# Kernel optimization log

Measured on AMD Instinct MI355X. Metric: run time of the kernel, lower is better.

## Reference

```python
import jax, jax.numpy as jnp
import numpy as np

HID = 256
DT = 0.05
B = 131072


def setup_inputs() -> dict:
    key = jax.random.key(0)
    ks = jax.random.split(key, 20)
    n = jax.random.normal
    inp = {
        "q": n(ks[0], (B, 1), jnp.float32),
        "p": n(ks[1], (B, 1), jnp.float32),
        "u": n(ks[2], (B, 1), jnp.float32),
        # kinetic MLP T(q_enc, p): in dim 3
        "kW1": n(ks[3], (HID, 3), jnp.float32) / np.sqrt(3.0),
        "kb1": n(ks[4], (HID,), jnp.float32) * 0.01,
        "kW2": n(ks[5], (HID, HID), jnp.float32) / np.sqrt(HID),
        "kb2": n(ks[6], (HID,), jnp.float32) * 0.01,
        "kW3": n(ks[7], (1, HID), jnp.float32) / np.sqrt(HID),
        "kb3": n(ks[8], (1,), jnp.float32) * 0.01,
        # potential MLP V(q_enc): in dim 2
        "pW1": n(ks[9], (HID, 2), jnp.float32) / np.sqrt(2.0),
        "pb1": n(ks[10], (HID,), jnp.float32) * 0.01,
        "pW2": n(ks[11], (HID, HID), jnp.float32) / np.sqrt(HID),
        "pb2": n(ks[12], (HID,), jnp.float32) * 0.01,
        "pW3": n(ks[13], (1, HID), jnp.float32) / np.sqrt(HID),
        "pb3": n(ks[14], (1,), jnp.float32) * 0.01,
        # learned structure matrices (std=0.01 as in nn.init.normal_)
        "A": n(ks[15], (2, 2), jnp.float32) * 0.01,
        "L_param": n(ks[16], (2, 2), jnp.float32) * 0.01,
        "b_ctrl": n(ks[17], (1, 1), jnp.float32) * 0.01,
    }
    return inp


def reference(q, p, u, kW1, kb1, kW2, kb2, kW3, kb3,
              pW1, pb1, pW2, pb2, pW3, pb3, A, L_param, b_ctrl):
    sp = jax.nn.softplus

    def H_sum(z):  # z: [B,2] -> scalar sum of H over batch
        q_, p_ = z[:, :1], z[:, 1:]
        enc = jnp.concatenate([jnp.sin(q_), jnp.cos(q_)], axis=-1)  # [B,2]
        x = jnp.concatenate([enc, p_], axis=-1)                      # [B,3]
        h = sp(x @ kW1.T + kb1)
        h = sp(h @ kW2.T + kb2)
        T = (h @ kW3.T + kb3)[:, 0]
        g = sp(enc @ pW1.T + pb1)
        g = sp(g @ pW2.T + pb2)
        V = (g @ pW3.T + pb3)[:, 0]
        return jnp.sum(T + V)

    # M = J - R with J = A - A^T, R = L L^T, L = strict-lower + softplus(diag)
    J = A - A.T
    L = jnp.tril(L_param, -1) + jnp.diag(sp(jnp.diagonal(L_param)))
    M = J - L @ L.T                          # [2,2]
    Bu = u @ b_ctrl.T                        # [B,1]
    zeros_q = jnp.zeros_like(q)

    def dyn(q_, p_):
        # torch detaches z before autograd.grad -> stop_gradient here
        z = jax.lax.stop_gradient(jnp.concatenate([q_, p_], axis=-1))
        gH = jax.grad(H_sum)(z)              # [B,2] = dH/dz per sample
        dz = gH @ M.T + jnp.concatenate([zeros_q, Bu], axis=-1)
        return dz[:, :1], dz[:, 1:]

    dt = DT
    dq1, dp1 = dyn(q, p)
    dq2, dp2 = dyn(q + 0.5 * dt * dq1, p + 0.5 * dt * dp1)
    dq3, dp3 = dyn(q + 0.5 * dt * dq2, p + 0.5 * dt * dp2)
    dq4, dp4 = dyn(q + dt * dq3, p + dt * dp3)
    q_next = q + dt / 6.0 * (dq1 + 2 * dq2 + 2 * dq3 + dq4)
    p_next = p + dt / 6.0 * (dp1 + 2 * dp2 + 2 * dp3 + dp4)
    return jnp.concatenate([q_next, p_next], axis=-1)  # [B,2]
```

## Files before the change

### kernel.cpp

```cpp
#include <hip/hip_runtime.h>

#define HID 256
#define BT 64
#define DTC 0.05f

typedef __attribute__((ext_vector_type(4))) float f32x4;
typedef __attribute__((ext_vector_type(8))) __bf16 bf16x8;

__device__ __forceinline__ unsigned cvt_pk_bf16(float lo, float hi) {
    unsigned r;
    asm("v_cvt_pk_bf16_f32 %0, %1, %2" : "=v"(r) : "v"(lo), "v"(hi));
    return r;
}

__device__ __forceinline__ unsigned short f2bf(float f) {
    unsigned int x = __float_as_uint(f);
    x += 0x7fffu + ((x >> 16) & 1u);
    return (unsigned short)(x >> 16);
}

__device__ __forceinline__ float sgpr_f(float v) {
    return __uint_as_float(__builtin_amdgcn_readfirstlane(__float_as_uint(v)));
}

#define OFF_FWDT 0
#define OFF_BWDT 65536
#define OFF_FWDV 131072
#define OFF_BWDV 196608
#define OFF_PROJT 262144
#define OFF_PROJV 266240
#define TOTAL_PRE 270336

__global__ void prepack_kernel(const float* __restrict__ kW1, const float* __restrict__ kW2,
                               const float* __restrict__ pW1, const float* __restrict__ pW2,
                               unsigned short* __restrict__ ws) {
    int t = blockIdx.x * 256 + threadIdx.x;
    if (t >= TOTAL_PRE) return;
    float v;
    if (t < OFF_FWDV) {
        int tt = t & 65535;
        bool bwd = t >= OFF_BWDT;
        int j = tt & 7, lane = (tt >> 3) & 63, kk = (tt >> 9) & 7, nt = tt >> 12;
        int n = nt * 16 + (lane & 15);
        int k = kk * 32 + (lane >> 4) * 8 + j;
        v = bwd ? kW2[k * HID + n] : kW2[n * HID + k];
    } else if (t < OFF_PROJT) {
        int tt = (t - OFF_FWDV) & 65535;
        bool bwd = t >= OFF_BWDV;
        int j = tt & 7, lane = (tt >> 3) & 63, kk = (tt >> 9) & 7, nt = tt >> 12;
        int n = nt * 16 + (lane & 15);
        int k = kk * 32 + (lane >> 4) * 8 + j;
        v = bwd ? pW2[k * HID + n] : pW2[n * HID + k];
    } else if (t < OFF_PROJV) {
        int tt = t - OFF_PROJT;
        int j = tt & 7, lane = (tt >> 3) & 63, kk = tt >> 9;
        int c = lane & 15;
        int k = kk * 32 + (lane >> 4) * 8 + j;
        v = (c < 3) ? kW1[k * 3 + c] : 0.f;
    } else {
        int tt = t - OFF_PROJV;
        int j = tt & 7, lane = (tt >> 3) & 63, kk = tt >> 9;
        int c = lane & 15;
        int k = kk * 32 + (lane >> 4) * 8 + j;
        v = (c < 2) ? pW1[k * 2 + c] : 0.f;
    }
    ws[t] = f2bf(v);
}


#define MFMA __builtin_amdgcn_mfma_f32_16x16x32_bf16

struct NetRegs { float w0[2], w1[2], w2[2], b1[2], b2[2], w3[2]; };

template <int IND, int NOUT>
__device__ __forceinline__ void run_net(
    char* bufAc, char* bufBc,
    const float* sh_sin, const float* sh_cos, const float* sh_pv,
    const NetRegs& R,
    const unsigned short* __restrict__ fwdB, const unsigned short* __restrict__ bwdB,
    const unsigned short* __restrict__ projB,
    float* g0, float* g1, float* g2,
    int w, int lane)
{
    const int lr = lane & 15;
    const int lg = lane >> 4;
    const unsigned int arx = (unsigned)(lr & 7) << 4;
    const unsigned int cbase = ((unsigned)lg << 4) ^ arx;

    unsigned s1p[16];

#pragma unroll
    for (int mt = 0; mt < 4; ++mt) {
#pragma unroll
        for (int r = 0; r < 4; ++r) {
            int row = mt * 16 + lg * 4 + r;
            float sv = sh_sin[row], cv = sh_cos[row];
            float pv = (IND == 3) ? sh_pv[row] : 0.f;
            unsigned int rowx = (unsigned)(row & 7) << 4;
            char* rowp = bufAc + row * 512;
            float sp[2], sg[2];
#pragma unroll
            for (int nt = 0; nt < 2; ++nt) {
                float x = fmaf(R.w0[nt], sv, R.b1[nt]);
                x = fmaf(R.w1[nt], cv, x);
                if (IND == 3) x = fmaf(R.w2[nt], pv, x);
                float e = __expf(-fabsf(x));
                sp[nt] = fmaxf(x, 0.f) + __logf(1.f + e);
                float t = __builtin_amdgcn_rcpf(1.f + e);
                sg[nt] = (x < 0.f) ? e * t : t;
            }
            unsigned d01 = cvt_pk_bf16(sp[0], sp[1]);
            int j0 = w * 32 + lr;
            *(unsigned short*)(rowp + (((j0 +  0) * 2) ^ rowx)) = (unsigned short)d01;
            *(unsigned short*)(rowp + (((j0 + 16) * 2) ^ rowx)) = (unsigned short)(d01 >> 16);
            s1p[mt * 4 + r] = cvt_pk_bf16(sg[0], sg[1]);
        }
    }

    const unsigned short* fb = fwdB + (w * 2) * 8 * 512 + lane * 8;
    bf16x8 c0 = *(const bf16x8*)(fb + 0 * 512);
    bf16x8 c1 = *(const bf16x8*)(fb + 8 * 512);
    __syncthreads();

    f32x4 acc[4][2];
#pragma unroll
    for (int mt = 0; mt < 4; ++mt)
#pragma unroll
        for (int nt = 0; nt < 2; ++nt)
            acc[mt][nt] = (f32x4){0.f, 0.f, 0.f, 0.f};
    {
#pragma unroll 1
        for (int kk = 0; kk < 8; ++kk) {
            unsigned int off = cbase ^ (unsigned)(kk << 6);
            bf16x8 af0 = *(const bf16x8*)(bufAc + (0 * 16 + lr) * 512 + off);
            bf16x8 af1 = *(const bf16x8*)(bufAc + (1 * 16 + lr) * 512 + off);
            bf16x8 af2 = *(const bf16x8*)(bufAc + (2 * 16 + lr) * 512 + off);
            bf16x8 af3 = *(const bf16x8*)(bufAc + (3 * 16 + lr) * 512 + off);
            acc[0][0] = MFMA(af0, c0, acc[0][0], 0, 0, 0);
            acc[0][1] = MFMA(af0, c1, acc[0][1], 0, 0, 0);
            acc[1][0] = MFMA(af1, c0, acc[1][0], 0, 0, 0);
            acc[1][1] = MFMA(af1, c1, acc[1][1], 0, 0, 0);
            acc[2][0] = MFMA(af2, c0, acc[2][0], 0, 0, 0);
            acc[2][1] = MFMA(af2, c1, acc[2][1], 0, 0, 0);
            acc[3][0] = MFMA(af3, c0, acc[3][0], 0, 0, 0);
            acc[3][1] = MFMA(af3, c1, acc[3][1], 0, 0, 0);
            if (kk < 7) {
                c0 = *(const bf16x8*)(fb + (0 * 8 + kk + 1) * 512);
                c1 = *(const bf16x8*)(fb + (1 * 8 + kk + 1) * 512);
            }
        }
    }

#pragma unroll
    for (int nt = 0; nt < 2; ++nt) {
        int i = w * 32 + nt * 16 + lr;
#pragma unroll
        for (int mt = 0; mt < 4; ++mt) {
            float val[4];
#pragma unroll
            for (int r = 0; r < 4; ++r) {
                float x = acc[mt][nt][r] + R.b2[nt];
                float e = __expf(-fabsf(x));
                float t = __builtin_amdgcn_rcpf(1.f + e);
                float sg = (x < 0.f) ? e * t : t;
                val[r] = R.w3[nt] * sg;
            }
            unsigned d01 = cvt_pk_bf16(val[0], val[1]);
            unsigned d23 = cvt_pk_bf16(val[2], val[3]);
#pragma unroll
            for (int r = 0; r < 4; ++r) {
                int row = mt * 16 + lg * 4 + r;
                unsigned short hv = (r == 0) ? (unsigned short)d01
                                  : (r == 1) ? (unsigned short)(d01 >> 16)
                                  : (r == 2) ? (unsigned short)d23
                                             : (unsigned short)(d23 >> 16);
                *(unsigned short*)(bufBc + row * 512 + ((i * 2) ^ ((unsigned)(row & 7) << 4))) = hv;
            }
        }
    }

    const unsigned short* bb = bwdB + (w * 2) * 8 * 512 + lane * 8;
    c0 = *(const bf16x8*)(bb + 0 * 512);
    c1 = *(const bf16x8*)(bb + 8 * 512);
    __syncthreads();

#pragma unroll
    for (int mt = 0; mt < 4; ++mt)
#pragma unroll
        for (int nt = 0; nt < 2; ++nt)
            acc[mt][nt] = (f32x4){0.f, 0.f, 0.f, 0.f};
    {
#pragma unroll 1
        for (int kk = 0; kk < 8; ++kk) {
            unsigned int off = cbase ^ (unsigned)(kk << 6);
            bf16x8 af0 = *(const bf16x8*)(bufBc + (0 * 16 + lr) * 512 + off);
            bf16x8 af1 = *(const bf16x8*)(bufBc + (1 * 16 + lr) * 512 + off);
            bf16x8 af2 = *(const bf16x8*)(bufBc + (2 * 16 + lr) * 512 + off);
            bf16x8 af3 = *(const bf16x8*)(bufBc + (3 * 16 + lr) * 512 + off);
            acc[0][0] = MFMA(af0, c0, acc[0][0], 0, 0, 0);
            acc[0][1] = MFMA(af0, c1, acc[0][1], 0, 0, 0);
            acc[1][0] = MFMA(af1, c0, acc[1][0], 0, 0, 0);
            acc[1][1] = MFMA(af1, c1, acc[1][1], 0, 0, 0);
            acc[2][0] = MFMA(af2, c0, acc[2][0], 0, 0, 0);
            acc[2][1] = MFMA(af2, c1, acc[2][1], 0, 0, 0);
            acc[3][0] = MFMA(af3, c0, acc[3][0], 0, 0, 0);
            acc[3][1] = MFMA(af3, c1, acc[3][1], 0, 0, 0);
            if (kk < 7) {
                c0 = *(const bf16x8*)(bb + (0 * 8 + kk + 1) * 512);
                c1 = *(const bf16x8*)(bb + (1 * 8 + kk + 1) * 512);
            }
        }
    }

#pragma unroll
    for (int mt = 0; mt < 4; ++mt) {
#pragma unroll
        for (int r = 0; r < 4; ++r) {
            int row = mt * 16 + lg * 4 + r;
            unsigned int rowx = (unsigned)(row & 7) << 4;
            char* rowp = bufAc + row * 512;
            unsigned pa = s1p[mt * 4 + r];
            float sg0 = __uint_as_float(pa << 16);
            float sg1 = __uint_as_float(pa & 0xffff0000u);
            unsigned d01 = cvt_pk_bf16(acc[mt][0][r] * sg0, acc[mt][1][r] * sg1);
            int j0 = w * 32 + lr;
            *(unsigned short*)(rowp + (((j0 +  0) * 2) ^ rowx)) = (unsigned short)d01;
            *(unsigned short*)(rowp + (((j0 + 16) * 2) ^ rowx)) = (unsigned short)(d01 >> 16);
        }
    }
    __syncthreads();

    if (w < 4) {
        const unsigned short* pb = projB + lane * 8;
        f32x4 pacc = (f32x4){0.f, 0.f, 0.f, 0.f};
        char* arow = bufAc + (w * 16 + lr) * 512;
#pragma unroll 1
        for (int kk = 0; kk < 8; ++kk) {
            bf16x8 bv = *(const bf16x8*)(pb + kk * 512);
            bf16x8 af = *(const bf16x8*)(arow + (cbase ^ (unsigned)(kk << 6)));
            pacc = MFMA(af, bv, pacc, 0, 0, 0);
        }
        if (lr < NOUT) {
            float* dst = (lr == 0) ? g0 : ((lr == 1) ? g1 : g2);
#pragma unroll
            for (int r = 0; r < 4; ++r) dst[w * 16 + lg * 4 + r] = pacc[r];
        }
    }
    __syncthreads();
}

__global__ __launch_bounds__(512, 2) void phgn_kernel(
    const float* __restrict__ q, const float* __restrict__ p, const float* __restrict__ u,
    const float* __restrict__ kW1, const float* __restrict__ kb1,
    const float* __restrict__ kb2, const float* __restrict__ kW3,
    const float* __restrict__ pW1, const float* __restrict__ pb1,
    const float* __restrict__ pb2, const float* __restrict__ pW3,
    const float* __restrict__ A, const float* __restrict__ Lp, const float* __restrict__ bctrl,
    const unsigned short* __restrict__ ws, float* __restrict__ out)
{
    __shared__ __attribute__((aligned(16))) unsigned short bufA[BT * HID];
    __shared__ __attribute__((aligned(16))) unsigned short bufB[BT * HID];
    __shared__ float sh_sin[BT], sh_cos[BT], sh_pv[BT];
    __shared__ float gx0[BT], gx1[BT], gx2[BT], ge0[BT], ge1[BT];

    const int tid = threadIdx.x;
    const int w = tid >> 6, lane = tid & 63;
    const int lr = lane & 15;
    const int base = blockIdx.x * BT;

    NetRegs RT, RV;
#pragma unroll
    for (int nt = 0; nt < 2; ++nt) {
        int j = w * 32 + nt * 16 + lr;
        RT.w0[nt] = kW1[j * 3 + 0];
        RT.w1[nt] = kW1[j * 3 + 1];
        RT.w2[nt] = kW1[j * 3 + 2];
        RT.b1[nt] = kb1[j];
        RT.b2[nt] = kb2[j];
        RT.w3[nt] = kW3[j];
        RV.w0[nt] = pW1[j * 2 + 0];
        RV.w1[nt] = pW1[j * 2 + 1];
        RV.w2[nt] = 0.f;
        RV.b1[nt] = pb1[j];
        RV.b2[nt] = pb2[j];
        RV.w3[nt] = pW3[j];
    }

    float l00 = __logf(1.f + __expf(Lp[0]));
    float l11 = __logf(1.f + __expf(Lp[3]));
    float l10 = Lp[2];
    float J01 = A[1] - A[2];
    float M00 = sgpr_f(-(l00 * l00));
    float M01 = sgpr_f(J01 - l00 * l10);
    float M10 = sgpr_f(-J01 - l10 * l00);
    float M11 = sgpr_f(-(l10 * l10 + l11 * l11));

    float q0 = 0.f, p0 = 0.f, buv = 0.f, aq = 0.f, ap = 0.f;
    if (tid < BT) {
        q0 = q[base + tid]; p0 = p[base + tid]; buv = u[base + tid] * bctrl[0];
        float s, c; __sincosf(q0, &s, &c);
        sh_sin[tid] = s; sh_cos[tid] = c; sh_pv[tid] = p0;
    }
    __syncthreads();

    char* bufAc = (char*)bufA;
    char* bufBc = (char*)bufB;
#pragma unroll 1
    for (int s = 0; s < 4; ++s) {
        run_net<3, 3>(bufAc, bufBc, sh_sin, sh_cos, sh_pv, RT,
                      ws + OFF_FWDT, ws + OFF_BWDT, ws + OFF_PROJT, gx0, gx1, gx2, w, lane);
        run_net<2, 2>(bufAc, bufBc, sh_sin, sh_cos, sh_pv, RV,
                      ws + OFF_FWDV, ws + OFF_BWDV, ws + OFF_PROJV, ge0, ge1, ge1, w, lane);
        if (tid < BT) {
            float gq = (gx0[tid] + ge0[tid]) * sh_cos[tid] - (gx1[tid] + ge1[tid]) * sh_sin[tid];
            float gp = gx2[tid];
            float dq = M00 * gq + M01 * gp;
            float dp = M10 * gq + M11 * gp + buv;
            float wgt = (s == 0 || s == 3) ? 1.f : 2.f;
            aq += wgt * dq; ap += wgt * dp;
            if (s < 3) {
                float cs = (s == 2) ? 1.f : 0.5f;
                float qs = fmaf(cs * DTC, dq, q0);
                float ps = fmaf(cs * DTC, dp, p0);
                float sn, cn; __sincosf(qs, &sn, &cn);
                sh_sin[tid] = sn; sh_cos[tid] = cn; sh_pv[tid] = ps;
            } else {
                float qn = fmaf(DTC / 6.f, aq, q0);
                float pn = fmaf(DTC / 6.f, ap, p0);
                ((float2*)out)[base + tid] = make_float2(qn, pn);
            }
        }
        __syncthreads();
    }
}

extern "C" void kernel_launch(void* const* d_in, const int* in_sizes, int n_in,
                              void* d_out, int out_size, void* d_ws, size_t ws_size,
                              hipStream_t stream) {
    const float* q    = (const float*)d_in[0];
    const float* p    = (const float*)d_in[1];
    const float* u    = (const float*)d_in[2];
    const float* kW1  = (const float*)d_in[3];
    const float* kb1  = (const float*)d_in[4];
    const float* kW2  = (const float*)d_in[5];
    const float* kb2  = (const float*)d_in[6];
    const float* kW3  = (const float*)d_in[7];
    const float* pW1  = (const float*)d_in[9];
    const float* pb1  = (const float*)d_in[10];
    const float* pW2  = (const float*)d_in[11];
    const float* pb2  = (const float*)d_in[12];
    const float* pW3  = (const float*)d_in[13];
    const float* A    = (const float*)d_in[15];
    const float* Lp   = (const float*)d_in[16];
    const float* bctl = (const float*)d_in[17];
    unsigned short* ws = (unsigned short*)d_ws;
    float* out = (float*)d_out;
    int B = in_sizes[0];

    prepack_kernel<<<(TOTAL_PRE + 255) / 256, 256, 0, stream>>>(kW1, kW2, pW1, pW2, ws);
    phgn_kernel<<<B / BT, 512, 0, stream>>>(q, p, u, kW1, kb1, kb2, kW3,
                                            pW1, pb1, pb2, pW3, A, Lp, bctl, ws, out);
}
```

Baseline: 715.2 us.

## Split batch rows across two wave groups with 1024-thread blocks

Doubles the block from 8 to 16 waves. Each wave now owns a 32-row by 32-column tile instead of 64 rows by 32 columns, with `wm` selecting the row half and `wn` the column slice. This halves per-wave accumulators and MFMA work and raises the resident wave count, to hide LDS and exp latency. In exchange, more waves contend at each `__syncthreads`, and the B fragments are loaded redundantly by both row groups. The tighter launch bounds may also force register spills or limit occupancy through the 64 KB of LDS per block.

```diff
diff --git a/kernel.cpp b/kernel.cpp
--- a/kernel.cpp
+++ b/kernel.cpp
@@ -80,20 +80,20 @@
     const unsigned short* __restrict__ fwdB, const unsigned short* __restrict__ bwdB,
     const unsigned short* __restrict__ projB,
     float* g0, float* g1, float* g2,
-    int w, int lane)
+    int wm, int wn, int w, int lane)
 {
     const int lr = lane & 15;
     const int lg = lane >> 4;
     const unsigned int arx = (unsigned)(lr & 7) << 4;
     const unsigned int cbase = ((unsigned)lg << 4) ^ arx;
 
-    unsigned s1p[16];
-
-#pragma unroll
-    for (int mt = 0; mt < 4; ++mt) {
+    unsigned s1p[8];
+
+#pragma unroll
+    for (int mt = 0; mt < 2; ++mt) {
 #pragma unroll
         for (int r = 0; r < 4; ++r) {
-            int row = mt * 16 + lg * 4 + r;
+            int row = wm * 32 + mt * 16 + lg * 4 + r;
             float sv = sh_sin[row], cv = sh_cos[row];
             float pv = (IND == 3) ? sh_pv[row] : 0.f;
             unsigned int rowx = (unsigned)(row & 7) << 4;
@@ -110,21 +110,21 @@
                 sg[nt] = (x < 0.f) ? e * t : t;
             }
             unsigned d01 = cvt_pk_bf16(sp[0], sp[1]);
-            int j0 = w * 32 + lr;
+            int j0 = wn * 32 + lr;
             *(unsigned short*)(rowp + (((j0 +  0) * 2) ^ rowx)) = (unsigned short)d01;
             *(unsigned short*)(rowp + (((j0 + 16) * 2) ^ rowx)) = (unsigned short)(d01 >> 16);
             s1p[mt * 4 + r] = cvt_pk_bf16(sg[0], sg[1]);
         }
     }
 
-    const unsigned short* fb = fwdB + (w * 2) * 8 * 512 + lane * 8;
+    const unsigned short* fb = fwdB + (wn * 2) * 8 * 512 + lane * 8;
     bf16x8 c0 = *(const bf16x8*)(fb + 0 * 512);
     bf16x8 c1 = *(const bf16x8*)(fb + 8 * 512);
     __syncthreads();
 
-    f32x4 acc[4][2];
-#pragma unroll
-    for (int mt = 0; mt < 4; ++mt)
+    f32x4 acc[2][2];
+#pragma unroll
+    for (int mt = 0; mt < 2; ++mt)
 #pragma unroll
         for (int nt = 0; nt < 2; ++nt)
             acc[mt][nt] = (f32x4){0.f, 0.f, 0.f, 0.f};
@@ -132,18 +132,12 @@
 #pragma unroll 1
         for (int kk = 0; kk < 8; ++kk) {
             unsigned int off = cbase ^ (unsigned)(kk << 6);
-            bf16x8 af0 = *(const bf16x8*)(bufAc + (0 * 16 + lr) * 512 + off);
-            bf16x8 af1 = *(const bf16x8*)(bufAc + (1 * 16 + lr) * 512 + off);
-            bf16x8 af2 = *(const bf16x8*)(bufAc + (2 * 16 + lr) * 512 + off);
-            bf16x8 af3 = *(const bf16x8*)(bufAc + (3 * 16 + lr) * 512 + off);
+            bf16x8 af0 = *(const bf16x8*)(bufAc + (wm * 32 +  0 + lr) * 512 + off);
+            bf16x8 af1 = *(const bf16x8*)(bufAc + (wm * 32 + 16 + lr) * 512 + off);
             acc[0][0] = MFMA(af0, c0, acc[0][0], 0, 0, 0);
             acc[0][1] = MFMA(af0, c1, acc[0][1], 0, 0, 0);
             acc[1][0] = MFMA(af1, c0, acc[1][0], 0, 0, 0);
             acc[1][1] = MFMA(af1, c1, acc[1][1], 0, 0, 0);
-            acc[2][0] = MFMA(af2, c0, acc[2][0], 0, 0, 0);
-            acc[2][1] = MFMA(af2, c1, acc[2][1], 0, 0, 0);
-            acc[3][0] = MFMA(af3, c0, acc[3][0], 0, 0, 0);
-            acc[3][1] = MFMA(af3, c1, acc[3][1], 0, 0, 0);
             if (kk < 7) {
                 c0 = *(const bf16x8*)(fb + (0 * 8 + kk + 1) * 512);
                 c1 = *(const bf16x8*)(fb + (1 * 8 + kk + 1) * 512);
@@ -153,9 +147,9 @@
 
 #pragma unroll
     for (int nt = 0; nt < 2; ++nt) {
-        int i = w * 32 + nt * 16 + lr;
-#pragma unroll
-        for (int mt = 0; mt < 4; ++mt) {
+        int i = wn * 32 + nt * 16 + lr;
+#pragma unroll
+        for (int mt = 0; mt < 2; ++mt) {
             float val[4];
 #pragma unroll
             for (int r = 0; r < 4; ++r) {
@@ -169,7 +163,7 @@
             unsigned d23 = cvt_pk_bf16(val[2], val[3]);
 #pragma unroll
             for (int r = 0; r < 4; ++r) {
-                int row = mt * 16 + lg * 4 + r;
+                int row = wm * 32 + mt * 16 + lg * 4 + r;
                 unsigned short hv = (r == 0) ? (unsigned short)d01
                                   : (r == 1) ? (unsigned short)(d01 >> 16)
                                   : (r == 2) ? (unsigned short)d23
@@ -179,13 +173,13 @@
         }
     }
 
-    const unsigned short* bb = bwdB + (w * 2) * 8 * 512 + lane * 8;
+    const unsigned short* bb = bwdB + (wn * 2) * 8 * 512 + lane * 8;
     c0 = *(const bf16x8*)(bb + 0 * 512);
     c1 = *(const bf16x8*)(bb + 8 * 512);
     __syncthreads();
 
 #pragma unroll
-    for (int mt = 0; mt < 4; ++mt)
+    for (int mt = 0; mt < 2; ++mt)
 #pragma unroll
         for (int nt = 0; nt < 2; ++nt)
             acc[mt][nt] = (f32x4){0.f, 0.f, 0.f, 0.f};
@@ -193,18 +187,12 @@
 #pragma unroll 1
         for (int kk = 0; kk < 8; ++kk) {
             unsigned int off = cbase ^ (unsigned)(kk << 6);
-            bf16x8 af0 = *(const bf16x8*)(bufBc + (0 * 16 + lr) * 512 + off);
-            bf16x8 af1 = *(const bf16x8*)(bufBc + (1 * 16 + lr) * 512 + off);
-            bf16x8 af2 = *(const bf16x8*)(bufBc + (2 * 16 + lr) * 512 + off);
-            bf16x8 af3 = *(const bf16x8*)(bufBc + (3 * 16 + lr) * 512 + off);
+            bf16x8 af0 = *(const bf16x8*)(bufBc + (wm * 32 +  0 + lr) * 512 + off);
+            bf16x8 af1 = *(const bf16x8*)(bufBc + (wm * 32 + 16 + lr) * 512 + off);
             acc[0][0] = MFMA(af0, c0, acc[0][0], 0, 0, 0);
             acc[0][1] = MFMA(af0, c1, acc[0][1], 0, 0, 0);
             acc[1][0] = MFMA(af1, c0, acc[1][0], 0, 0, 0);
             acc[1][1] = MFMA(af1, c1, acc[1][1], 0, 0, 0);
-            acc[2][0] = MFMA(af2, c0, acc[2][0], 0, 0, 0);
-            acc[2][1] = MFMA(af2, c1, acc[2][1], 0, 0, 0);
-            acc[3][0] = MFMA(af3, c0, acc[3][0], 0, 0, 0);
-            acc[3][1] = MFMA(af3, c1, acc[3][1], 0, 0, 0);
             if (kk < 7) {
                 c0 = *(const bf16x8*)(bb + (0 * 8 + kk + 1) * 512);
                 c1 = *(const bf16x8*)(bb + (1 * 8 + kk + 1) * 512);
@@ -213,17 +201,17 @@
     }
 
 #pragma unroll
-    for (int mt = 0; mt < 4; ++mt) {
+    for (int mt = 0; mt < 2; ++mt) {
 #pragma unroll
         for (int r = 0; r < 4; ++r) {
-            int row = mt * 16 + lg * 4 + r;
+            int row = wm * 32 + mt * 16 + lg * 4 + r;
             unsigned int rowx = (unsigned)(row & 7) << 4;
             char* rowp = bufAc + row * 512;
             unsigned pa = s1p[mt * 4 + r];
             float sg0 = __uint_as_float(pa << 16);
             float sg1 = __uint_as_float(pa & 0xffff0000u);
             unsigned d01 = cvt_pk_bf16(acc[mt][0][r] * sg0, acc[mt][1][r] * sg1);
-            int j0 = w * 32 + lr;
+            int j0 = wn * 32 + lr;
             *(unsigned short*)(rowp + (((j0 +  0) * 2) ^ rowx)) = (unsigned short)d01;
             *(unsigned short*)(rowp + (((j0 + 16) * 2) ^ rowx)) = (unsigned short)(d01 >> 16);
         }
@@ -249,7 +237,7 @@
     __syncthreads();
 }
 
-__global__ __launch_bounds__(512, 2) void phgn_kernel(
+__global__ __launch_bounds__(1024, 4) void phgn_kernel(
     const float* __restrict__ q, const float* __restrict__ p, const float* __restrict__ u,
     const float* __restrict__ kW1, const float* __restrict__ kb1,
     const float* __restrict__ kb2, const float* __restrict__ kW3,
@@ -265,13 +253,14 @@
 
     const int tid = threadIdx.x;
     const int w = tid >> 6, lane = tid & 63;
+    const int wm = w >> 3, wn = w & 7;
     const int lr = lane & 15;
     const int base = blockIdx.x * BT;
 
     NetRegs RT, RV;
 #pragma unroll
     for (int nt = 0; nt < 2; ++nt) {
-        int j = w * 32 + nt * 16 + lr;
+        int j = wn * 32 + nt * 16 + lr;
         RT.w0[nt] = kW1[j * 3 + 0];
         RT.w1[nt] = kW1[j * 3 + 1];
         RT.w2[nt] = kW1[j * 3 + 2];
@@ -308,9 +297,9 @@
 #pragma unroll 1
     for (int s = 0; s < 4; ++s) {
         run_net<3, 3>(bufAc, bufBc, sh_sin, sh_cos, sh_pv, RT,
-                      ws + OFF_FWDT, ws + OFF_BWDT, ws + OFF_PROJT, gx0, gx1, gx2, w, lane);
+                      ws + OFF_FWDT, ws + OFF_BWDT, ws + OFF_PROJT, gx0, gx1, gx2, wm, wn, w, lane);
         run_net<2, 2>(bufAc, bufBc, sh_sin, sh_cos, sh_pv, RV,
-                      ws + OFF_FWDV, ws + OFF_BWDV, ws + OFF_PROJV, ge0, ge1, ge1, w, lane);
+                      ws + OFF_FWDV, ws + OFF_BWDV, ws + OFF_PROJV, ge0, ge1, ge1, wm, wn, w, lane);
         if (tid < BT) {
             float gq = (gx0[tid] + ge0[tid]) * sh_cos[tid] - (gx1[tid] + ge1[tid]) * sh_sin[tid];
             float gp = gx2[tid];
@@ -358,6 +347,6 @@
     int B = in_sizes[0];
 
     prepack_kernel<<<(TOTAL_PRE + 255) / 256, 256, 0, stream>>>(kW1, kW2, pW1, pW2, ws);
-    phgn_kernel<<<B / BT, 512, 0, stream>>>(q, p, u, kW1, kb1, kb2, kW3,
-                                            pW1, pb1, pb2, pW3, A, Lp, bctl, ws, out);
-}
+    phgn_kernel<<<B / BT, 1024, 0, stream>>>(q, p, u, kW1, kb1, kb2, kW3,
+                                             pW1, pb1, pb2, pW3, A, Lp, bctl, ws, out);
+}
```

Result: slower. 807.2 us (+12.9%).

## Permute K dimension in prepacked weights to enable packed 32-bit LDS stores

Applied to the files above, without the earlier changes.

Reorders the K index in the prepacked weight layouts so that each lane's two hidden columns (j and j+16) sit adjacent in the activation rows. The three LDS writes of activations can then store one 32-bit packed bf16 pair instead of two 16-bit halves, halving LDS store instructions. The per-row sin/cos/p loads also become 16-byte vector reads from aligned shared arrays. The permutation must stay consistent across all MFMA operand layouts, which adds correctness risk.

```diff
diff --git a/kernel.cpp b/kernel.cpp
--- a/kernel.cpp
+++ b/kernel.cpp
@@ -42,26 +42,30 @@
         bool bwd = t >= OFF_BWDT;
         int j = tt & 7, lane = (tt >> 3) & 63, kk = (tt >> 9) & 7, nt = tt >> 12;
         int n = nt * 16 + (lane & 15);
-        int k = kk * 32 + (lane >> 4) * 8 + j;
+        int p = (lane >> 4) * 8 + j;
+        int k = kk * 32 + ((p & 1) << 4) + (p >> 1);
         v = bwd ? kW2[k * HID + n] : kW2[n * HID + k];
     } else if (t < OFF_PROJT) {
         int tt = (t - OFF_FWDV) & 65535;
         bool bwd = t >= OFF_BWDV;
         int j = tt & 7, lane = (tt >> 3) & 63, kk = (tt >> 9) & 7, nt = tt >> 12;
         int n = nt * 16 + (lane & 15);
-        int k = kk * 32 + (lane >> 4) * 8 + j;
+        int p = (lane >> 4) * 8 + j;
+        int k = kk * 32 + ((p & 1) << 4) + (p >> 1);
         v = bwd ? pW2[k * HID + n] : pW2[n * HID + k];
     } else if (t < OFF_PROJV) {
         int tt = t - OFF_PROJT;
         int j = tt & 7, lane = (tt >> 3) & 63, kk = tt >> 9;
         int c = lane & 15;
-        int k = kk * 32 + (lane >> 4) * 8 + j;
+        int p = (lane >> 4) * 8 + j;
+        int k = kk * 32 + ((p & 1) << 4) + (p >> 1);
         v = (c < 3) ? kW1[k * 3 + c] : 0.f;
     } else {
         int tt = t - OFF_PROJV;
         int j = tt & 7, lane = (tt >> 3) & 63, kk = tt >> 9;
         int c = lane & 15;
-        int k = kk * 32 + (lane >> 4) * 8 + j;
+        int p = (lane >> 4) * 8 + j;
+        int k = kk * 32 + ((p & 1) << 4) + (p >> 1);
         v = (c < 2) ? pW1[k * 2 + c] : 0.f;
     }
     ws[t] = f2bf(v);
@@ -86,18 +90,21 @@
     const int lg = lane >> 4;
     const unsigned int arx = (unsigned)(lr & 7) << 4;
     const unsigned int cbase = ((unsigned)lg << 4) ^ arx;
+    const unsigned int colb = (unsigned)(w * 64 + lr * 4);
 
     unsigned s1p[16];
 
 #pragma unroll
     for (int mt = 0; mt < 4; ++mt) {
+        int r0 = mt * 16 + lg * 4;
+        f32x4 sv4 = *(const f32x4*)&sh_sin[r0];
+        f32x4 cv4 = *(const f32x4*)&sh_cos[r0];
+        f32x4 pv4 = *(const f32x4*)&sh_pv[r0];
 #pragma unroll
         for (int r = 0; r < 4; ++r) {
-            int row = mt * 16 + lg * 4 + r;
-            float sv = sh_sin[row], cv = sh_cos[row];
-            float pv = (IND == 3) ? sh_pv[row] : 0.f;
-            unsigned int rowx = (unsigned)(row & 7) << 4;
-            char* rowp = bufAc + row * 512;
+            int row = r0 + r;
+            float sv = sv4[r], cv = cv4[r];
+            float pv = (IND == 3) ? pv4[r] : 0.f;
             float sp[2], sg[2];
 #pragma unroll
             for (int nt = 0; nt < 2; ++nt) {
@@ -109,11 +116,9 @@
                 float t = __builtin_amdgcn_rcpf(1.f + e);
                 sg[nt] = (x < 0.f) ? e * t : t;
             }
-            unsigned d01 = cvt_pk_bf16(sp[0], sp[1]);
-            int j0 = w * 32 + lr;
-            *(unsigned short*)(rowp + (((j0 +  0) * 2) ^ rowx)) = (unsigned short)d01;
-            *(unsigned short*)(rowp + (((j0 + 16) * 2) ^ rowx)) = (unsigned short)(d01 >> 16);
+            unsigned dsp = cvt_pk_bf16(sp[0], sp[1]);
             s1p[mt * 4 + r] = cvt_pk_bf16(sg[0], sg[1]);
+            *(unsigned*)(bufAc + row * 512 + (colb ^ ((unsigned)(row & 7) << 4))) = dsp;
         }
     }
 
@@ -152,30 +157,20 @@
     }
 
 #pragma unroll
-    for (int nt = 0; nt < 2; ++nt) {
-        int i = w * 32 + nt * 16 + lr;
-#pragma unroll
-        for (int mt = 0; mt < 4; ++mt) {
-            float val[4];
-#pragma unroll
-            for (int r = 0; r < 4; ++r) {
-                float x = acc[mt][nt][r] + R.b2[nt];
-                float e = __expf(-fabsf(x));
-                float t = __builtin_amdgcn_rcpf(1.f + e);
-                float sg = (x < 0.f) ? e * t : t;
-                val[r] = R.w3[nt] * sg;
-            }
-            unsigned d01 = cvt_pk_bf16(val[0], val[1]);
-            unsigned d23 = cvt_pk_bf16(val[2], val[3]);
-#pragma unroll
-            for (int r = 0; r < 4; ++r) {
-                int row = mt * 16 + lg * 4 + r;
-                unsigned short hv = (r == 0) ? (unsigned short)d01
-                                  : (r == 1) ? (unsigned short)(d01 >> 16)
-                                  : (r == 2) ? (unsigned short)d23
-                                             : (unsigned short)(d23 >> 16);
-                *(unsigned short*)(bufBc + row * 512 + ((i * 2) ^ ((unsigned)(row & 7) << 4))) = hv;
-            }
+    for (int mt = 0; mt < 4; ++mt) {
+#pragma unroll
+        for (int r = 0; r < 4; ++r) {
+            float x0 = acc[mt][0][r] + R.b2[0];
+            float x1 = acc[mt][1][r] + R.b2[1];
+            float e0 = __expf(-fabsf(x0));
+            float t0 = __builtin_amdgcn_rcpf(1.f + e0);
+            float s0 = (x0 < 0.f) ? e0 * t0 : t0;
+            float e1 = __expf(-fabsf(x1));
+            float t1 = __builtin_amdgcn_rcpf(1.f + e1);
+            float s1 = (x1 < 0.f) ? e1 * t1 : t1;
+            unsigned d = cvt_pk_bf16(R.w3[0] * s0, R.w3[1] * s1);
+            int row = mt * 16 + lg * 4 + r;
+            *(unsigned*)(bufBc + row * 512 + (colb ^ ((unsigned)(row & 7) << 4))) = d;
         }
     }
 
@@ -217,15 +212,11 @@
 #pragma unroll
         for (int r = 0; r < 4; ++r) {
             int row = mt * 16 + lg * 4 + r;
-            unsigned int rowx = (unsigned)(row & 7) << 4;
-            char* rowp = bufAc + row * 512;
             unsigned pa = s1p[mt * 4 + r];
             float sg0 = __uint_as_float(pa << 16);
             float sg1 = __uint_as_float(pa & 0xffff0000u);
-            unsigned d01 = cvt_pk_bf16(acc[mt][0][r] * sg0, acc[mt][1][r] * sg1);
-            int j0 = w * 32 + lr;
-            *(unsigned short*)(rowp + (((j0 +  0) * 2) ^ rowx)) = (unsigned short)d01;
-            *(unsigned short*)(rowp + (((j0 + 16) * 2) ^ rowx)) = (unsigned short)(d01 >> 16);
+            unsigned d = cvt_pk_bf16(acc[mt][0][r] * sg0, acc[mt][1][r] * sg1);
+            *(unsigned*)(bufAc + row * 512 + (colb ^ ((unsigned)(row & 7) << 4))) = d;
         }
     }
     __syncthreads();
@@ -260,7 +251,9 @@
 {
     __shared__ __attribute__((aligned(16))) unsigned short bufA[BT * HID];
     __shared__ __attribute__((aligned(16))) unsigned short bufB[BT * HID];
-    __shared__ float sh_sin[BT], sh_cos[BT], sh_pv[BT];
+    __shared__ __attribute__((aligned(16))) float sh_sin[BT];
+    __shared__ __attribute__((aligned(16))) float sh_cos[BT];
+    __shared__ __attribute__((aligned(16))) float sh_pv[BT];
     __shared__ float gx0[BT], gx1[BT], gx2[BT], ge0[BT], ge1[BT];
 
     const int tid = threadIdx.x;
```

Measured after the change: 663.6 us. 7.2% less time.
